# Kernel tuning notes

Hardware: AMD Instinct MI355X
Metric: run time of the kernel (lower is better)

## Reference

```python
import jax, jax.numpy as jnp
import numpy as np

# hyperparams (match CombinedPeakLoss defaults)
ALPHA, BETA, GAMMA, DELTA, EPSILON = 1.0, 2.0, 1.0, 0.5, 0.5
PEAK_WINDOW = 2
DAYTIME_WEIGHT = 2.0
TEMPERATURE = 0.1
HOURS = 24
NEG = -1e9


def setup_inputs() -> dict:
    key = jax.random.key(0)
    k1, k2 = jax.random.split(key)
    B, S = 16384, 720  # 30 days of hourly data
    y_pred = jax.random.uniform(k1, (B, S), dtype=jnp.float32)
    y_true = jax.random.uniform(k2, (B, S), dtype=jnp.float32)
    return {"y_pred": y_pred, "y_true": y_true}


def _soft_peaks(y_bdh, day_mask, hours):
    # y_bdh: [B,D,H]; day_mask: [1,D,H] bool; hours: [H]
    masked = jnp.where(day_mask, y_bdh, NEG)
    attn = jax.nn.softmax(masked / TEMPERATURE, axis=-1)  # [B,D,H]
    peak_val = (attn * y_bdh).sum(-1)                      # [B,D]
    peak_time = (attn * hours).sum(-1)                     # [B,D]
    return peak_val, peak_time


def reference(y_pred, y_true):
    B, S = y_true.shape
    D = S // HOURS
    dt = y_true.dtype

    # default is_daytime: tiled hour-of-day, daytime = 6..20 inclusive
    t = jnp.tile(jnp.arange(HOURS), D)[:S]                 # [S]
    is_day = ((t >= 6) & (t <= 20))                        # [S] bool
    day_mask = is_day.reshape(1, D, HOURS)                 # [1,D,H]
    hours = jnp.arange(HOURS, dtype=dt)                    # [H]

    yt = y_true.reshape(B, D, HOURS)
    yp = y_pred.reshape(B, D, HOURS)

    # L_overall
    L_overall = jnp.mean((y_pred - y_true) ** 2)

    # soft peak extraction for both true and pred
    t_pv, t_pt = _soft_peaks(yt, day_mask, hours)
    p_pv, p_pt = _soft_peaks(yp, day_mask, hours)
    L_peak_value = jnp.mean((p_pv - t_pv) ** 2)
    L_peak_time = jnp.mean((p_pt - t_pt) ** 2)

    # peak shape loss: hard argmax on daytime-masked truth, windowed normalized MSE
    masked_true = jnp.where(day_mask, yt, NEG)
    peak_idx = jnp.argmax(masked_true, axis=-1)            # [B,D]
    ws = jnp.maximum(0, peak_idx - PEAK_WINDOW)            # [B,D]
    we = jnp.minimum(HOURS, peak_idx + PEAK_WINDOW + 1)    # [B,D]
    h = jnp.arange(HOURS)
    wmask = (h[None, None, :] >= ws[..., None]) & (h[None, None, :] < we[..., None])  # [B,D,H]
    tmax = jnp.max(jnp.where(wmask, yt, NEG), axis=-1)     # [B,D]
    pmax = jnp.max(jnp.where(wmask, yp, NEG), axis=-1)     # [B,D]
    valid = tmax > 1e-6
    tmax_safe = jnp.where(valid, tmax, 1.0)
    diff = yp / (pmax[..., None] + 1e-6) - yt / tmax_safe[..., None]
    wlen = (we - ws).astype(dt)
    mse_win = jnp.sum(jnp.where(wmask, diff ** 2, 0.0), axis=-1) / wlen  # [B,D]
    L_peak_shape = jnp.sum(jnp.where(valid, mse_win, 0.0)) / (jnp.sum(valid) + 1e-6)

    # daytime-weighted extra MSE
    dw = jnp.where(is_day, DAYTIME_WEIGHT, 1.0).astype(dt)  # [S]
    weighted_mse = jnp.mean((y_pred - y_true) ** 2 * dw)
    L_daytime = weighted_mse - L_overall

    total = (ALPHA * L_overall + BETA * L_peak_value + GAMMA * L_peak_time
             + DELTA * L_peak_shape + EPSILON * L_daytime)
    return total
```

## Files before the change

### kernel.cpp

```cpp
#include <hip/hip_runtime.h>

#define HOURS 24
#define RPB 256
#define PSTR 25


__global__ __launch_bounds__(256) void peakloss_main(
    const float* __restrict__ ypred, const float* __restrict__ ytrue,
    float* __restrict__ partials, int nrows, int nblocks) {
  __shared__ float lt[RPB * PSTR];
  __shared__ float lp[RPB * PSTR];

  const int tid = threadIdx.x;
  const int tile0 = blockIdx.x * RPB;
  const int rows = min(RPB, nrows - tile0);

  if (rows == RPB) {
    const float4* t4 = (const float4*)(ytrue + (size_t)tile0 * HOURS);
    const float4* p4 = (const float4*)(ypred + (size_t)tile0 * HOURS);
#pragma unroll
    for (int j = 0; j < 6; ++j) {
      int f4 = tid + j * 256;
      float4 a = t4[f4];
      float4 b = p4[f4];
      int d0 = f4 * 4;
      float av[4] = {a.x, a.y, a.z, a.w};
      float bv[4] = {b.x, b.y, b.z, b.w};
#pragma unroll
      for (int c = 0; c < 4; ++c) {
        int d = d0 + c;
        int pa = d + d / HOURS;
        lt[pa] = av[c];
        lp[pa] = bv[c];
      }
    }
  } else {
    for (int d = tid; d < rows * HOURS; d += 256) {
      int pa = d + d / HOURS;
      lt[pa] = ytrue[(size_t)tile0 * HOURS + d];
      lp[pa] = ypred[(size_t)tile0 * HOURS + d];
    }
  }
  __syncthreads();

  float s_sq = 0.f, s_day = 0.f, s_pv = 0.f, s_pt = 0.f, s_shape = 0.f, s_valid = 0.f;

  if (tid < rows) {
    const float* tr = lt + tid * PSTR;
    const float* pr = lp + tid * PSTR;

    float mt = -1e30f, mp = -1e30f;
    int idx = 6;
#pragma unroll
    for (int h = 0; h < HOURS; ++h) {
      float th = tr[h], ph = pr[h];
      float d = ph - th;
      float dd = d * d;
      s_sq += dd;
      if (h >= 6 && h <= 20) {
        s_day += dd;
        if (th > mt) { mt = th; idx = h; }
        mp = fmaxf(mp, ph);
      }
    }

    int ws = idx - 2;
    float den_t = 0.f, nv_t = 0.f, nt_t = 0.f;
    float den_p = 0.f, nv_p = 0.f, nt_p = 0.f;
    float tmax = -1e30f, pmax = -1e30f;
#pragma unroll
    for (int h = 4; h <= 22; ++h) {
      float th = tr[h], ph = pr[h];
      if (h >= 6 && h <= 20) {
        float et = __expf((th - mt) * 10.f);
        den_t += et; nv_t += et * th; nt_t += et * (float)h;
        float ep = __expf((ph - mp) * 10.f);
        den_p += ep; nv_p += ep * ph; nt_p += ep * (float)h;
      }
      bool in = (h >= ws) & (h < ws + 5);
      if (in) { tmax = fmaxf(tmax, th); pmax = fmaxf(pmax, ph); }
    }
    float r_t = __builtin_amdgcn_rcpf(den_t);
    float r_p = __builtin_amdgcn_rcpf(den_p);
    float dv  = nv_p * r_p - nv_t * r_t;
    float dtm = nt_p * r_p - nt_t * r_t;
    s_pv += dv * dv;
    s_pt += dtm * dtm;

    bool valid = tmax > 1e-6f;
    float tms = valid ? tmax : 1.0f;
    float r_tms  = __builtin_amdgcn_rcpf(tms);
    float r_pden = __builtin_amdgcn_rcpf(pmax + 1e-6f);
    float a = 0.f;
#pragma unroll
    for (int h = 4; h <= 22; ++h) {
      bool in = (h >= ws) & (h < ws + 5);
      float d = pr[h] * r_pden - tr[h] * r_tms;
      a += in ? d * d : 0.f;
    }
    if (valid) { s_shape += a * 0.2f; s_valid += 1.0f; }
  }

  float v[6] = {s_sq, s_day, s_pv, s_pt, s_shape, s_valid};
#pragma unroll
  for (int j = 0; j < 6; ++j) {
#pragma unroll
    for (int off = 32; off >= 1; off >>= 1) v[j] += __shfl_down(v[j], off, 64);
  }
  __shared__ float red[6][4];
  int lane = threadIdx.x & 63, wave = threadIdx.x >> 6;
  __syncthreads();
  if (lane == 0) {
#pragma unroll
    for (int j = 0; j < 6; ++j) red[j][wave] = v[j];
  }
  __syncthreads();
  if (threadIdx.x < 6) {
    int j = threadIdx.x;
    partials[(size_t)j * nblocks + blockIdx.x] =
        red[j][0] + red[j][1] + red[j][2] + red[j][3];
  }
}

__global__ __launch_bounds__(256) void peakloss_reduce(
    const float* __restrict__ partials, float* __restrict__ out,
    int nblocks, double inv_BS, double inv_BD) {
  double s[6] = {0, 0, 0, 0, 0, 0};
  for (int i = threadIdx.x; i < nblocks; i += 256) {
#pragma unroll
    for (int j = 0; j < 6; ++j) s[j] += (double)partials[(size_t)j * nblocks + i];
  }
#pragma unroll
  for (int j = 0; j < 6; ++j) {
#pragma unroll
    for (int off = 32; off >= 1; off >>= 1) s[j] += __shfl_down(s[j], off, 64);
  }
  __shared__ double red[6][4];
  int lane = threadIdx.x & 63, wave = threadIdx.x >> 6;
  if (lane == 0) {
#pragma unroll
    for (int j = 0; j < 6; ++j) red[j][wave] = s[j];
  }
  __syncthreads();
  if (threadIdx.x == 0) {
    double a[6];
#pragma unroll
    for (int j = 0; j < 6; ++j)
      a[j] = red[j][0] + red[j][1] + red[j][2] + red[j][3];
    double L_overall = a[0] * inv_BS;
    double L_day     = a[1] * inv_BS;
    double L_pv      = a[2] * inv_BD;
    double L_pt      = a[3] * inv_BD;
    double L_shape   = a[4] / (a[5] + 1e-6);
    out[0] = (float)(L_overall + 2.0 * L_pv + L_pt + 0.5 * L_shape + 0.5 * L_day);
  }
}

extern "C" void kernel_launch(void* const* d_in, const int* in_sizes, int n_in,
                              void* d_out, int out_size, void* d_ws, size_t ws_size,
                              hipStream_t stream) {
  const float* ypred = (const float*)d_in[0];
  const float* ytrue = (const float*)d_in[1];
  float* out = (float*)d_out;
  float* partials = (float*)d_ws;

  long long N = in_sizes[0];
  int nrows = (int)(N / HOURS);
  int grid = (nrows + RPB - 1) / RPB;

  peakloss_main<<<grid, 256, 0, stream>>>(ypred, ytrue, partials, nrows, grid);

  double inv_BS = 1.0 / (double)N;
  double inv_BD = 1.0 / (double)nrows;
  peakloss_reduce<<<1, 256, 0, stream>>>(partials, out, grid, inv_BS, inv_BD);
}
```

Baseline: 26.73 us.

## Load rows directly into registers and expand windowed shape MSE algebraically

Drops the LDS staging tile and has each thread read its own 24-float row of both inputs straight into registers with six float4 loads each. The second pass over the peak window is replaced by sums of t², p² and t·p gathered in the first pass, from which the normalized MSE is rebuilt algebraically. This removes the shared-memory round trip, one barrier and a loop. In exchange, each thread's float4 loads now stride 96 bytes apart across the wavefront instead of being contiguous, and the expanded form can lose precision through cancellation.

```diff
diff --git a/kernel.cpp b/kernel.cpp
--- a/kernel.cpp
+++ b/kernel.cpp
@@ -1,66 +1,42 @@
 #include <hip/hip_runtime.h>
 
 #define HOURS 24
-#define RPB 256
-#define PSTR 25
 
 
 __global__ __launch_bounds__(256) void peakloss_main(
     const float* __restrict__ ypred, const float* __restrict__ ytrue,
     float* __restrict__ partials, int nrows, int nblocks) {
-  __shared__ float lt[RPB * PSTR];
-  __shared__ float lp[RPB * PSTR];
-
   const int tid = threadIdx.x;
-  const int tile0 = blockIdx.x * RPB;
-  const int rows = min(RPB, nrows - tile0);
-
-  if (rows == RPB) {
-    const float4* t4 = (const float4*)(ytrue + (size_t)tile0 * HOURS);
-    const float4* p4 = (const float4*)(ypred + (size_t)tile0 * HOURS);
-#pragma unroll
-    for (int j = 0; j < 6; ++j) {
-      int f4 = tid + j * 256;
-      float4 a = t4[f4];
-      float4 b = p4[f4];
-      int d0 = f4 * 4;
-      float av[4] = {a.x, a.y, a.z, a.w};
-      float bv[4] = {b.x, b.y, b.z, b.w};
-#pragma unroll
-      for (int c = 0; c < 4; ++c) {
-        int d = d0 + c;
-        int pa = d + d / HOURS;
-        lt[pa] = av[c];
-        lp[pa] = bv[c];
-      }
-    }
-  } else {
-    for (int d = tid; d < rows * HOURS; d += 256) {
-      int pa = d + d / HOURS;
-      lt[pa] = ytrue[(size_t)tile0 * HOURS + d];
-      lp[pa] = ypred[(size_t)tile0 * HOURS + d];
-    }
-  }
-  __syncthreads();
+  const int r = blockIdx.x * 256 + tid;
 
   float s_sq = 0.f, s_day = 0.f, s_pv = 0.f, s_pt = 0.f, s_shape = 0.f, s_valid = 0.f;
 
-  if (tid < rows) {
-    const float* tr = lt + tid * PSTR;
-    const float* pr = lp + tid * PSTR;
+  if (r < nrows) {
+    float t[HOURS], p[HOURS];
+    const float4* t4 = (const float4*)(ytrue + (size_t)r * HOURS);
+    const float4* p4 = (const float4*)(ypred + (size_t)r * HOURS);
+#pragma unroll
+    for (int k = 0; k < 6; ++k) {
+      float4 a = t4[k];
+      t[4 * k + 0] = a.x; t[4 * k + 1] = a.y; t[4 * k + 2] = a.z; t[4 * k + 3] = a.w;
+    }
+#pragma unroll
+    for (int k = 0; k < 6; ++k) {
+      float4 b = p4[k];
+      p[4 * k + 0] = b.x; p[4 * k + 1] = b.y; p[4 * k + 2] = b.z; p[4 * k + 3] = b.w;
+    }
 
     float mt = -1e30f, mp = -1e30f;
     int idx = 6;
 #pragma unroll
     for (int h = 0; h < HOURS; ++h) {
-      float th = tr[h], ph = pr[h];
-      float d = ph - th;
+      float d = p[h] - t[h];
       float dd = d * d;
       s_sq += dd;
       if (h >= 6 && h <= 20) {
         s_day += dd;
-        if (th > mt) { mt = th; idx = h; }
-        mp = fmaxf(mp, ph);
+        if (t[h] > mt) { mt = t[h]; idx = h; }
+        mp = fmaxf(mp, p[h]);
       }
     }
 
@@ -68,9 +44,10 @@
     float den_t = 0.f, nv_t = 0.f, nt_t = 0.f;
     float den_p = 0.f, nv_p = 0.f, nt_p = 0.f;
     float tmax = -1e30f, pmax = -1e30f;
+    float St2 = 0.f, Sp2 = 0.f, Stp = 0.f;
 #pragma unroll
     for (int h = 4; h <= 22; ++h) {
-      float th = tr[h], ph = pr[h];
+      float th = t[h], ph = p[h];
       if (h >= 6 && h <= 20) {
         float et = __expf((th - mt) * 10.f);
         den_t += et; nv_t += et * th; nt_t += et * (float)h;
@@ -78,7 +55,10 @@
         den_p += ep; nv_p += ep * ph; nt_p += ep * (float)h;
       }
       bool in = (h >= ws) & (h < ws + 5);
-      if (in) { tmax = fmaxf(tmax, th); pmax = fmaxf(pmax, ph); }
+      if (in) {
+        tmax = fmaxf(tmax, th); pmax = fmaxf(pmax, ph);
+        St2 += th * th; Sp2 += ph * ph; Stp += th * ph;
+      }
     }
     float r_t = __builtin_amdgcn_rcpf(den_t);
     float r_p = __builtin_amdgcn_rcpf(den_p);
@@ -89,16 +69,10 @@
 
     bool valid = tmax > 1e-6f;
     float tms = valid ? tmax : 1.0f;
-    float r_tms  = __builtin_amdgcn_rcpf(tms);
-    float r_pden = __builtin_amdgcn_rcpf(pmax + 1e-6f);
-    float a = 0.f;
-#pragma unroll
-    for (int h = 4; h <= 22; ++h) {
-      bool in = (h >= ws) & (h < ws + 5);
-      float d = pr[h] * r_pden - tr[h] * r_tms;
-      a += in ? d * d : 0.f;
-    }
-    if (valid) { s_shape += a * 0.2f; s_valid += 1.0f; }
+    float rt = __builtin_amdgcn_rcpf(tms);
+    float rp = __builtin_amdgcn_rcpf(pmax + 1e-6f);
+    float aa = rp * rp * Sp2 + rt * rt * St2 - 2.f * rp * rt * Stp;
+    if (valid) { s_shape += aa * 0.2f; s_valid += 1.0f; }
   }
 
   float v[6] = {s_sq, s_day, s_pv, s_pt, s_shape, s_valid};
@@ -109,7 +83,6 @@
   }
   __shared__ float red[6][4];
   int lane = threadIdx.x & 63, wave = threadIdx.x >> 6;
-  __syncthreads();
   if (lane == 0) {
 #pragma unroll
     for (int j = 0; j < 6; ++j) red[j][wave] = v[j];
@@ -166,7 +139,7 @@
 
   long long N = in_sizes[0];
   int nrows = (int)(N / HOURS);
-  int grid = (nrows + RPB - 1) / RPB;
+  int grid = (nrows + 255) / 256;
 
   peakloss_main<<<grid, 256, 0, stream>>>(ypred, ytrue, partials, nrows, grid);
 
```

New measurement: 26.32 us. About the same (-1.5%).
